# Optimization experiments

Measured on AMD Instinct MI355X. Metric: run time of the kernel, lower is better.

## Reference

```python
import jax, jax.numpy as jnp
import numpy as np

STRIDES = (8, 16, 32, 64, 128)
POOL = 7
IMG = 1024.0


def _crop_and_resize(fm, boxes, box_ids, crop_h, crop_w):
    """tf.image.crop_and_resize semantics (bilinear, extrapolation_value=0).
    fm: [B,H,W,C] channels-last; boxes: [N,4] normalized (y1,x1,y2,x2); box_ids: [N] int.
    Returns [N,crop_h,crop_w,C]."""
    B, H, W, C = fm.shape
    y1, x1, y2, x2 = boxes[:, 0], boxes[:, 1], boxes[:, 2], boxes[:, 3]
    fy = jnp.arange(crop_h, dtype=boxes.dtype) / (crop_h - 1)
    fx = jnp.arange(crop_w, dtype=boxes.dtype) / (crop_w - 1)
    ys = (y1[:, None] + (y2 - y1)[:, None] * fy) * (H - 1)   # [N,crop_h]
    xs = (x1[:, None] + (x2 - x1)[:, None] * fx) * (W - 1)   # [N,crop_w]
    y0f = jnp.floor(ys)
    x0f = jnp.floor(xs)
    wy = (ys - y0f)[:, :, None, None]
    wx = (xs - x0f)[:, None, :, None]
    y0 = jnp.clip(y0f, 0, H - 1).astype(jnp.int32)
    y1i = jnp.clip(y0f + 1, 0, H - 1).astype(jnp.int32)
    x0 = jnp.clip(x0f, 0, W - 1).astype(jnp.int32)
    x1i = jnp.clip(x0f + 1, 0, W - 1).astype(jnp.int32)
    b = box_ids[:, None, None]
    gather = lambda yi, xi: fm[b, yi[:, :, None], xi[:, None, :]]  # [N,ch,cw,C]
    top = gather(y0, x0) * (1 - wx) + gather(y0, x1i) * wx
    bot = gather(y1i, x0) * (1 - wx) + gather(y1i, x1i) * wx
    out = top * (1 - wy) + bot * wy
    valid = ((ys >= 0) & (ys <= H - 1))[:, :, None] & ((xs >= 0) & (xs <= W - 1))[:, None, :]
    return jnp.where(valid[..., None], out, jnp.zeros((), out.dtype))


def reference(batch_gt_boxes, fm0, fm1, fm2, fm3, fm4):
    boxes = batch_gt_boxes[..., :4]
    B, N, _ = boxes.shape
    box_ids = jnp.repeat(jnp.arange(B, dtype=jnp.int32), N)  # [B*N]
    boxes = boxes.reshape(-1, 4)
    # trim_padding_boxes: inputs contain no all-zero (padding) boxes, so all kept.
    rois_from_fms = []
    for fm, s in zip((fm0, fm1, fm2, fm3, fm4), STRIDES):
        H, W = fm.shape[1], fm.shape[2]
        # normalize_boxes: pixel coords -> feature-map coords (/stride) -> [0,1]
        scale = jnp.array([s * (H - 1), s * (W - 1), s * (H - 1), s * (W - 1)],
                          dtype=boxes.dtype)
        normed = boxes / scale
        rois_from_fms.append(_crop_and_resize(fm, normed, box_ids, POOL, POOL))
    rois = jnp.concatenate(rois_from_fms, axis=-1)  # [B*N, 7, 7, 5*C]
    return rois, box_ids


def setup_inputs() -> dict:
    key = jax.random.key(0)
    ks = jax.random.split(key, 6)
    u = jax.random.uniform(ks[0], (8, 100, 4), dtype=jnp.float32) * IMG
    ya, xa, yb, xb = u[..., 0], u[..., 1], u[..., 2], u[..., 3]
    # valid, non-degenerate, non-zero boxes (so trim_padding_boxes keeps all)
    batch_gt_boxes = jnp.stack([
        jnp.minimum(ya, yb), jnp.minimum(xa, xb),
        jnp.maximum(ya, yb) + 1.0, jnp.maximum(xa, xb) + 1.0], axis=-1)
    fms = {}
    for i, s in enumerate(STRIDES):
        hw = int(IMG) // s
        fms[f"fm{i}"] = jax.random.normal(ks[i + 1], (8, hw, hw, 256), dtype=jnp.float32)
    return {"batch_gt_boxes": batch_gt_boxes, **fms}
```

## Files before the change

### kernel.cpp

```cpp
#include <hip/hip_runtime.h>

#define NCH 256
#define ROIS_ELEMS 50176000

typedef float vf4 __attribute__((ext_vector_type(4)));

__global__ __launch_bounds__(256) void roi_cell_kernel(
    const float* __restrict__ boxes,
    const float* __restrict__ fm0,
    const float* __restrict__ fm1,
    const float* __restrict__ fm2,
    const float* __restrict__ fm3,
    const float* __restrict__ fm4,
    float* __restrict__ out,
    float* __restrict__ out_ids)
{
    const int wave = threadIdx.x >> 6;
    const int lane = threadIdx.x & 63;

    const int bswz = (blockIdx.x & 7) * 1225 + (blockIdx.x >> 3);
    const int cell = bswz * 4 + wave;

    const int n   = cell / 49;
    const int rem = cell - n * 49;
    const int py  = rem / 7;
    const int px  = rem - py * 7;

    const float* fms[5] = { fm0, fm1, fm2, fm3, fm4 };

    const int img = n / 100;
    const float y1 = boxes[n * 4 + 0];
    const float x1 = boxes[n * 4 + 1];
    const float y2 = boxes[n * 4 + 2];
    const float x2 = boxes[n * 4 + 3];

    const float fy = __fdiv_rn((float)py, 6.0f);
    const float fx = __fdiv_rn((float)px, 6.0f);

    float wy_[5], owy_[5], wx_[5], owx_[5];
    bool  vv_[5];
    int o00[5], o01[5], o10[5], o11[5];
    #pragma unroll
    for (int l = 0; l < 5; ++l) {
        const int   H    = 128 >> l;
        const float Hm1  = (float)(H - 1);
        const float scale = (float)((8 << l) * (H - 1));

        const float y1n = __fdiv_rn(y1, scale);
        const float y2n = __fdiv_rn(y2, scale);
        const float x1n = __fdiv_rn(x1, scale);
        const float x2n = __fdiv_rn(x2, scale);

        const float ys = __fmul_rn(__fadd_rn(y1n, __fmul_rn(__fsub_rn(y2n, y1n), fy)), Hm1);
        const float xs = __fmul_rn(__fadd_rn(x1n, __fmul_rn(__fsub_rn(x2n, x1n), fx)), Hm1);
        vv_[l] = (ys >= 0.0f) && (ys <= Hm1) && (xs >= 0.0f) && (xs <= Hm1);

        const float y0f = floorf(ys);
        const float x0f = floorf(xs);
        wy_[l] = ys - y0f;  owy_[l] = 1.0f - wy_[l];
        wx_[l] = xs - x0f;  owx_[l] = 1.0f - wx_[l];

        const int y0  = (int)fminf(fmaxf(y0f,        0.0f), Hm1);
        const int y1i = (int)fminf(fmaxf(y0f + 1.0f, 0.0f), Hm1);
        const int x0  = (int)fminf(fmaxf(x0f,        0.0f), Hm1);
        const int x1i = (int)fminf(fmaxf(x0f + 1.0f, 0.0f), Hm1);

        const int rowT = (img * H + y0 ) * H;
        const int rowB = (img * H + y1i) * H;
        o00[l] = __builtin_amdgcn_readfirstlane((rowT + x0 ) * NCH);
        o01[l] = __builtin_amdgcn_readfirstlane((rowT + x1i) * NCH);
        o10[l] = __builtin_amdgcn_readfirstlane((rowB + x0 ) * NCH);
        o11[l] = __builtin_amdgcn_readfirstlane((rowB + x1i) * NCH);
    }

    vf4 v00[5], v01[5], v10[5], v11[5];
    #pragma unroll
    for (int l = 0; l < 5; ++l) {
        const float* fm = fms[l];
        v00[l] = ((const vf4*)(fm + o00[l]))[lane];
        v01[l] = ((const vf4*)(fm + o01[l]))[lane];
        v10[l] = ((const vf4*)(fm + o10[l]))[lane];
        v11[l] = ((const vf4*)(fm + o11[l]))[lane];
    }

    float* obase = out + cell * 1280;
    #pragma unroll
    for (int l = 0; l < 5; ++l) {
        vf4 r = (v00[l] * owx_[l] + v01[l] * wx_[l]) * owy_[l]
              + (v10[l] * owx_[l] + v11[l] * wx_[l]) * wy_[l];
        if (!vv_[l]) { r = (vf4)0.0f; }
        __builtin_nontemporal_store(r, ((vf4*)(obase + l * NCH)) + lane);
    }

    if (rem == 0 && lane == 0) {
        out_ids[n] = (float)img;
    }
}

extern "C" void kernel_launch(void* const* d_in, const int* in_sizes, int n_in,
                              void* d_out, int out_size, void* d_ws, size_t ws_size,
                              hipStream_t stream) {
    const float* boxes = (const float*)d_in[0];
    const float* fm0   = (const float*)d_in[1];
    const float* fm1   = (const float*)d_in[2];
    const float* fm2   = (const float*)d_in[3];
    const float* fm3   = (const float*)d_in[4];
    const float* fm4   = (const float*)d_in[5];

    float* out     = (float*)d_out;
    float* out_ids = out + ROIS_ELEMS;

    roi_cell_kernel<<<9800, 256, 0, stream>>>(boxes, fm0, fm1, fm2, fm3, fm4, out, out_ids);
}
```

Measured before the change: 66.09 us.

## Process boxes in order of vertical center to improve feature-map cache locality

Each block ranks the 100 boxes of its image by y1+y2 in shared memory with an O(N^2) rank sort. It then maps its cells to boxes in that sorted order, so neighbouring blocks gather from nearby feature-map rows, which is meant to raise L2/MALL hit rates on the bilinear gathers. Outputs are still written to the original box positions. This adds redundant per-block sorting work, two barriers, and a less sequential output write pattern.

```diff
diff --git a/kernel.cpp b/kernel.cpp
--- a/kernel.cpp
+++ b/kernel.cpp
@@ -19,16 +19,38 @@
     const int lane = threadIdx.x & 63;
 
     const int bswz = (blockIdx.x & 7) * 1225 + (blockIdx.x >> 3);
-    const int cell = bswz * 4 + wave;
+    const int simg = bswz / 1225;
 
-    const int n   = cell / 49;
-    const int rem = cell - n * 49;
-    const int py  = rem / 7;
-    const int px  = rem - py * 7;
+    __shared__ float sy[100];
+    __shared__ int   inv[100];
+    const int t = threadIdx.x;
+    if (t < 100) {
+        const float* bb = boxes + (simg * 100 + t) * 4;
+        sy[t] = bb[0] + bb[2];
+    }
+    __syncthreads();
+    if (t < 100) {
+        const float my = sy[t];
+        int r = 0;
+        for (int j = 0; j < 100; ++j) {
+            const float o = sy[j];
+            r += (o < my || (o == my && j < t)) ? 1 : 0;
+        }
+        inv[r] = t;
+    }
+    __syncthreads();
+
+    const int cellS  = bswz * 4 + wave;
+    const int within = cellS - simg * 4900;
+    const int sIdx   = within / 49;
+    const int rem    = within - sIdx * 49;
+    const int py     = rem / 7;
+    const int px     = rem - py * 7;
+    const int n      = simg * 100 + inv[sIdx];
+    const int img    = simg;
 
     const float* fms[5] = { fm0, fm1, fm2, fm3, fm4 };
 
-    const int img = n / 100;
     const float y1 = boxes[n * 4 + 0];
     const float x1 = boxes[n * 4 + 1];
     const float y2 = boxes[n * 4 + 2];
@@ -83,7 +105,7 @@
         v11[l] = ((const vf4*)(fm + o11[l]))[lane];
     }
 
-    float* obase = out + cell * 1280;
+    float* obase = out + (n * 49 + rem) * 1280;
     #pragma unroll
     for (int l = 0; l < 5; ++l) {
         vf4 r = (v00[l] * owx_[l] + v01[l] * wx_[l]) * owy_[l]
```

Measured after the change: 66.66 us. Within noise of the previous version (+0.9%).
